# Optimization experiments

Hardware: AMD Instinct MI355X
Metric: run time of the kernel (lower is better)

Reference implementation:

```python
import jax, jax.numpy as jnp
import numpy as np
from jax import lax

ORDER = 6
WN = 0.5 / 50.0          # highpass_cutoff / (orig_fs/2)
UP, DOWN = 16, 25        # 64/100 reduced by gcd 4 (scipy resample_poly)
HALF_LEN = 10 * DOWN     # scipy kaiser half length = 10*max_rate
NTAPS = 2 * HALF_LEN + 1
PADLEN = 21              # sosfiltfilt default: 3*(2*n_sections+1), 3 biquads
CHANNELS = np.array([126, 125, 48, 112, 67, 93, 10, 61, 39, 108])
D_MODEL = 16
LN_EPS = 1e-5


def _butter_hp_sos(order, wn):
    # scipy.signal.butter(order, wn, btype='high', output='sos') in pure numpy
    fs = 2.0
    warped = 2.0 * fs * np.tan(np.pi * wn / fs)
    m = np.arange(-order + 1, order, 2)
    p = -np.exp(1j * np.pi * m / (2 * order))     # analog LP prototype poles
    k = np.real(1.0 / np.prod(-p))                # lp2hp gain (no zeros)
    p = warped / p                                # lp2hp poles; zeros at s=0
    z = np.zeros(order)
    fs2 = 2.0 * fs                                # bilinear, fs=2
    k = k * np.real(np.prod(fs2 - z) / np.prod(fs2 - p))
    z = (fs2 + z) / (fs2 - z)                     # digital zeros, all +1
    p = (fs2 + p) / (fs2 - p)
    pp = p[np.imag(p) > 0]
    pp = pp[np.argsort(-np.abs(np.abs(pp) - 1.0))]  # closest to unit circle last
    sos = []
    for i, pi in enumerate(pp):
        b = np.array([1.0, -2.0, 1.0]) * (k if i == 0 else 1.0)
        a = np.array([1.0, -2.0 * pi.real, np.abs(pi) ** 2])
        sos.append(np.concatenate([b, a]))
    return np.array(sos)


def _sosfilt_zi(sos):
    # scipy.signal.sosfilt_zi: steady-state of step response per section
    n = sos.shape[0]
    zi = np.zeros((n, 2))
    scale = 1.0
    for s in range(n):
        b0, b1, b2, _, a1, a2 = sos[s]
        A = np.array([[1.0 + a1, -1.0], [a2, 1.0]])
        B = np.array([b1 - a1 * b0, b2 - a2 * b0])
        zi[s] = scale * np.linalg.solve(A, B)
        scale *= (b0 + b1 + b2) / (1.0 + a1 + a2)
    return zi


SOS = _butter_hp_sos(ORDER, WN)
ZI = _sosfilt_zi(SOS)


def _resample_fir():
    # scipy firwin(2*half_len+1, 1/max_rate, window=('kaiser',5.0)) * up
    fc = 1.0 / DOWN
    m = np.arange(NTAPS) - (NTAPS - 1) / 2.0
    h = fc * np.sinc(fc * m) * np.kaiser(NTAPS, 5.0)
    h /= h.sum()
    return h * UP


H_BASE = _resample_fir()


def _pos_encoding(max_len, d):
    pos = np.arange(max_len)[:, None].astype(np.float64)
    div = np.exp(np.arange(0, d, 2) * (-np.log(10000.0) / d))
    pe = np.zeros((max_len, d))
    pe[:, 0::2] = np.sin(pos * div)
    pe[:, 1::2] = np.cos(pos * div)
    return pe.astype(np.float32)


PE = _pos_encoding(3840, D_MODEL)


def _sosfilt(x, zi):
    # x: (N,T), zi: (N,3,2). Cascade of biquads, transposed direct form II.
    sos = jnp.asarray(SOS, x.dtype)
    nsec = SOS.shape[0]

    def step(z, xt):
        v = xt
        zs = []
        for s in range(nsec):  # fixed tiny cascade, unrolled inside scan
            b0, b1, b2, a1, a2 = sos[s, 0], sos[s, 1], sos[s, 2], sos[s, 4], sos[s, 5]
            y = b0 * v + z[s][0]
            zs.append((b1 * v - a1 * y + z[s][1], b2 * v - a2 * y))
            v = y
        return tuple(zs), v

    z0 = tuple((zi[:, s, 0], zi[:, s, 1]) for s in range(nsec))
    _, y = lax.scan(step, z0, x.T)
    return y.T


def _sosfiltfilt(x):
    # scipy.signal.sosfiltfilt with default odd padding, padlen=21
    zi = jnp.asarray(ZI, x.dtype)
    front = 2.0 * x[:, :1] - x[:, PADLEN:0:-1]
    back = 2.0 * x[:, -1:] - x[:, -2:-PADLEN - 2:-1]
    ext = jnp.concatenate([front, x, back], axis=1)
    y = _sosfilt(ext, zi[None] * ext[:, 0, None, None])
    y = y[:, ::-1]
    y = _sosfilt(y, zi[None] * y[:, 0, None, None])
    return y[:, ::-1][:, PADLEN:-PADLEN]


def _resample_poly(x):
    # scipy.signal.resample_poly(x, 64, 100): upfirdn via dilated conv
    T = x.shape[-1]
    n_out = (T * UP) // DOWN + int((T * UP) % DOWN != 0)
    n_pre_pad = DOWN - HALF_LEN % DOWN
    n_pre_remove = (HALF_LEN + n_pre_pad) // DOWN

    def outlen(lh):
        return (((T - 1) * UP + lh) - 1) // DOWN + 1

    n_post = 0
    while outlen(NTAPS + n_pre_pad + n_post) < n_out + n_pre_remove:
        n_post += 1
    h = np.concatenate([np.zeros(n_pre_pad), H_BASE, np.zeros(n_post)])
    L = h.size
    rhs = jnp.asarray(h[::-1].copy(), x.dtype).reshape(1, 1, L)
    y = lax.conv_general_dilated(x[:, None, :], rhs, window_strides=(DOWN,),
                                 padding=[(L - 1, L - 1)], lhs_dilation=(UP,),
                                 dimension_numbers=('NCH', 'OIH', 'NCH'))
    return y[:, 0, n_pre_remove:n_pre_remove + n_out]


def _ln(x, g, b):
    mu = x.mean(-1, keepdims=True)
    var = ((x - mu) ** 2).mean(-1, keepdims=True)
    return (x - mu) * lax.rsqrt(var + LN_EPS) * g + b


def setup_inputs() -> dict:
    key = jax.random.key(0)
    ks = jax.random.split(key, 20)
    f32 = jnp.float32
    d = {
        'x': jax.random.normal(ks[0], (64, 128, 2000), f32),
        'conv_w': jax.random.normal(ks[1], (16, 10, 3), f32) * 0.15,
        'conv_b': jnp.zeros((16,), f32),
        'ln0_g': jnp.ones((16,), f32), 'ln0_b': jnp.zeros((16,), f32),
        'wqkv': jax.random.normal(ks[2], (48, 16), f32) * 0.125,
        'bqkv': jnp.zeros((48,), f32),
        'wo': jax.random.normal(ks[3], (16, 16), f32) * 0.25,
        'bo': jnp.zeros((16,), f32),
        'w1': jax.random.normal(ks[4], (32, 16), f32) * 0.2,
        'b1': jnp.zeros((32,), f32),
        'w2': jax.random.normal(ks[5], (16, 32), f32) * 0.2,
        'b2': jnp.zeros((16,), f32),
        'ln1_g': jnp.ones((16,), f32), 'ln1_b': jnp.zeros((16,), f32),
        'ln2_g': jnp.ones((16,), f32), 'ln2_b': jnp.zeros((16,), f32),
        'wfc': jax.random.normal(ks[6], (1, 16), f32) * 0.3,
        'bfc': jnp.zeros((1,), f32),
    }
    return d


def reference(x, conv_w, conv_b, ln0_g, ln0_b, wqkv, bqkv, wo, bo,
              w1, b1, w2, b2, ln1_g, ln1_b, ln2_g, ln2_b, wfc, bfc):
    B = x.shape[0]
    # remove Cz (last channel) then gather interesting channels
    x = x[:, :-1, :][:, jnp.asarray(CHANNELS), :]        # (B,10,T)
    x = x - x.mean(axis=1, keepdims=True)                # CAR
    C, T = x.shape[1], x.shape[2]
    xf = _sosfiltfilt(x.reshape(B * C, T))               # zero-phase highpass
    xr = _resample_poly(xf)                              # 100 Hz -> 64 Hz
    x = xr.reshape(B, C, -1)
    x = jnp.tanh(x)                                      # artifact_scale = 1.0
    mean = x.mean(axis=2, keepdims=True)                 # zscore, unbiased std
    var = ((x - mean) ** 2).sum(axis=2, keepdims=True) / (x.shape[2] - 1)
    std = jnp.maximum(jnp.sqrt(var), 1e-6)
    x = (x - mean) / std
    # conv1d k=3 pad=1 (10 -> 16) + relu
    x = lax.conv_general_dilated(x, conv_w, (1,), [(1, 1)],
                                 dimension_numbers=('NCH', 'OIH', 'NCH'))
    x = jax.nn.relu(x + conv_b[None, :, None])
    x = x.transpose(0, 2, 1)                             # (B,S,16)
    x = _ln(x, ln0_g, ln0_b)
    x = x + jnp.asarray(PE[:x.shape[1]], x.dtype)[None]
    # TransformerEncoderLayer, post-norm, nhead=1, relu FFN (eval: no dropout)
    qkv = x @ wqkv.T + bqkv
    q, k, v = jnp.split(qkv, 3, axis=-1)
    att = jax.nn.softmax(jnp.einsum('bqd,bkd->bqk', q, k) * 0.25, axis=-1)
    a = jnp.einsum('bqk,bkd->bqd', att, v) @ wo.T + bo
    x = _ln(x + a, ln1_g, ln1_b)
    f = jax.nn.relu(x @ w1.T + b1) @ w2.T + b2
    x = _ln(x + f, ln2_g, ln2_b)
    pooled = x.mean(axis=1)                              # adaptive avg pool -> 1
    return pooled @ wfc.T + bfc                          # (B,1)
```

## Files before the change

### kernel.cpp

```cpp
#include <hip/hip_runtime.h>
#include <cmath>
#include <complex>
#include <algorithm>

#ifndef M_PI
#define M_PI 3.14159265358979323846
#endif

typedef _Float16 f16x8 __attribute__((ext_vector_type(8)));
typedef _Float16 f16x4 __attribute__((ext_vector_type(4)));
typedef float f32x4 __attribute__((ext_vector_type(4)));

struct FiltArg {
  double b0[3], b1[3], b2[3], a1[3], a2[3];
  double zi0[3], zi1[3];
};
struct CorArg { double CA[32 * 6]; };
struct EigArg {
  double Pm[36], Pinv[36];
  double czi[6];
  double lam_re[3], lam_im[3];
  double lami_re[3], lami_im[3];
};
struct FirArg { float h[526]; };

static void design_sos(FiltArg& sa) {
  const int order = 6;
  const double wn = 0.5 / 50.0;
  const double fs = 2.0;
  double warped = 2.0 * fs * std::tan(M_PI * wn / fs);
  std::complex<double> p[6];
  for (int i = 0; i < order; i++) {
    int m = -order + 1 + 2 * i;
    p[i] = -std::exp(std::complex<double>(0.0, M_PI * m / (2.0 * order)));
  }
  std::complex<double> prod1(1, 0);
  for (int i = 0; i < 6; i++) prod1 *= -p[i];
  double k = (1.0 / prod1).real();
  for (int i = 0; i < 6; i++) p[i] = warped / p[i];
  const double fs2 = 2.0 * fs;
  std::complex<double> num(1, 0), den(1, 0);
  for (int i = 0; i < 6; i++) { num *= fs2; den *= (fs2 - p[i]); }
  k *= (num / den).real();
  for (int i = 0; i < 6; i++) p[i] = (fs2 + p[i]) / (fs2 - p[i]);
  std::complex<double> pp[3]; int n = 0;
  for (int i = 0; i < 6; i++) if (p[i].imag() > 0) pp[n++] = p[i];
  std::stable_sort(pp, pp + 3,
    [](const std::complex<double>& A, const std::complex<double>& B) {
      return std::fabs(std::abs(A) - 1.0) > std::fabs(std::abs(B) - 1.0);
    });
  double sos[3][6];
  for (int s = 0; s < 3; s++) {
    double g = (s == 0) ? k : 1.0;
    sos[s][0] = g; sos[s][1] = -2.0 * g; sos[s][2] = g;
    sos[s][3] = 1.0; sos[s][4] = -2.0 * pp[s].real(); sos[s][5] = std::norm(pp[s]);
  }
  double scale = 1.0;
  for (int s = 0; s < 3; s++) {
    double b0 = sos[s][0], b1 = sos[s][1], b2 = sos[s][2];
    double a1 = sos[s][4], a2 = sos[s][5];
    double det = 1.0 + a1 + a2;
    double r0 = b1 - a1 * b0, r1 = b2 - a2 * b0;
    double z0 = (r0 + r1) / det;
    double z1 = ((1.0 + a1) * r1 - a2 * r0) / det;
    sa.b0[s] = b0; sa.b1[s] = b1; sa.b2[s] = b2; sa.a1[s] = a1; sa.a2[s] = a2;
    sa.zi0[s] = scale * z0; sa.zi1[s] = scale * z1;
    scale *= (b0 + b1 + b2) / (1.0 + a1 + a2);
  }
}

static double host_step(const FiltArg& c, double z[6], double v) {
  for (int s = 0; s < 3; s++) {
    double y = c.b0[s] * v + z[2 * s];
    z[2 * s]     = c.b1[s] * v - c.a1[s] * y + z[2 * s + 1];
    z[2 * s + 1] = c.b2[s] * v - c.a2[s] * y;
    v = y;
  }
  return v;
}

static void build_filt(FiltArg& c, CorArg& co) {
  design_sos(c);
  for (int j = 0; j < 6; j++) {
    double z[6] = {0, 0, 0, 0, 0, 0};
    z[j] = 1.0;
    for (int i = 0; i < 32; i++) co.CA[i * 6 + j] = host_step(c, z, 0.0);
  }
}

static void build_eig(const FiltArg& c, EigArg& e) {
  double Pr[36];
  for (int s = 0; s < 3; s++) {
    double a1 = c.a1[s], a2 = c.a2[s];
    std::complex<double> disc = std::sqrt(std::complex<double>(a1 * a1 - 4.0 * a2, 0.0));
    std::complex<double> p = (-a1 + disc) / 2.0;
    if (p.imag() < 0) p = std::conj(p);
    std::complex<double> v[6] = {0, 0, 0, 0, 0, 0};
    v[2 * s] = 1.0;
    v[2 * s + 1] = a1 + p;
    std::complex<double> y = 1.0;
    for (int j = s + 1; j < 3; j++) {
      double b0j = c.b0[j], b1j = c.b1[j], b2j = c.b2[j];
      double a1j = c.a1[j], a2j = c.a2[j];
      std::complex<double> det = p * p + a1j * p + a2j;
      std::complex<double> r0 = (b1j - a1j * b0j) * y;
      std::complex<double> r1 = (b2j - a2j * b0j) * y;
      std::complex<double> z0 = (p * r0 + r1) / det;
      std::complex<double> z1 = ((p + a1j) * r1 - a2j * r0) / det;
      v[2 * j] = z0; v[2 * j + 1] = z1;
      y = b0j * y + z0;
    }
    for (int i = 0; i < 6; i++) {
      Pr[i * 6 + 2 * s]     = v[i].real();
      Pr[i * 6 + 2 * s + 1] = v[i].imag();
    }
    std::complex<double> lam = std::pow(p, 32);
    e.lam_re[s] = lam.real(); e.lam_im[s] = lam.imag();
    std::complex<double> li = 1.0 / lam;
    e.lami_re[s] = li.real(); e.lami_im[s] = li.imag();
  }
  for (int i = 0; i < 36; i++) e.Pm[i] = Pr[i];
  double M[6][12];
  for (int i = 0; i < 6; i++)
    for (int j = 0; j < 6; j++) { M[i][j] = Pr[i * 6 + j]; M[i][6 + j] = (i == j) ? 1.0 : 0.0; }
  for (int col = 0; col < 6; col++) {
    int piv = col;
    for (int i = col + 1; i < 6; i++)
      if (std::fabs(M[i][col]) > std::fabs(M[piv][col])) piv = i;
    if (piv != col) for (int j = 0; j < 12; j++) std::swap(M[col][j], M[piv][j]);
    double d = M[col][col];
    for (int j = 0; j < 12; j++) M[col][j] /= d;
    for (int i = 0; i < 6; i++) if (i != col) {
      double f = M[i][col];
      for (int j = 0; j < 12; j++) M[i][j] -= f * M[col][j];
    }
  }
  for (int i = 0; i < 6; i++)
    for (int j = 0; j < 6; j++) e.Pinv[i * 6 + j] = M[i][6 + j];
  double zv[6];
  for (int s = 0; s < 3; s++) { zv[2 * s] = c.zi0[s]; zv[2 * s + 1] = c.zi1[s]; }
  for (int i = 0; i < 6; i++) {
    double sum = 0.0;
    for (int j = 0; j < 6; j++) sum += e.Pinv[i * 6 + j] * zv[j];
    e.czi[i] = sum;
  }
}

static double bessel_i0(double x) {
  double s = 1.0, t = 1.0;
  for (int k = 1; k < 64; k++) {
    double u = x / (2.0 * k);
    t *= u * u; s += t;
    if (t < 1e-18 * s) break;
  }
  return s;
}

static void design_fir(FirArg& fa) {
  double h[501];
  const double fc = 1.0 / 25.0;
  double denom = bessel_i0(5.0);
  double sum = 0.0;
  for (int nn = 0; nn < 501; nn++) {
    double m = nn - 250.0;
    double xx = fc * m;
    double snc = (nn == 250) ? 1.0 : std::sin(M_PI * xx) / (M_PI * xx);
    double r = (2.0 * nn) / 500.0 - 1.0;
    double w = bessel_i0(5.0 * std::sqrt(std::max(0.0, 1.0 - r * r))) / denom;
    h[nn] = fc * snc * w; sum += h[nn];
  }
  for (int nn = 0; nn < 25; nn++) fa.h[nn] = 0.0f;
  for (int nn = 0; nn < 501; nn++) fa.h[25 + nn] = (float)(h[nn] / sum * 16.0);
}

__device__ inline double waveReduceSum(double v) {
  #pragma unroll
  for (int off = 32; off > 0; off >>= 1) v += __shfl_down(v, off, 64);
  return v;
}

__device__ inline void cpow_int(double br, double bi, int n, double& rr_, double& ri_) {
  double rr = 1.0, ri = 0.0;
  while (n) {
    if (n & 1) { double t = rr * br - ri * bi; ri = rr * bi + ri * br; rr = t; }
    double t2 = br * br - bi * bi; bi = 2.0 * br * bi; br = t2;
    n >>= 1;
  }
  rr_ = rr; ri_ = ri;
}

__global__ __launch_bounds__(256) void k_chansel_pe(const float* __restrict__ x,
                                                    float* __restrict__ xs,
                                                    float* __restrict__ pe,
                                                    float* __restrict__ out) {
  int gid = blockIdx.x;
  if (gid < 500) {
    int idx = gid * 256 + threadIdx.x;
    int b = idx / 2000, t = idx % 2000;
    const int ch[10] = {126, 125, 48, 112, 67, 93, 10, 61, 39, 108};
    const float* xb = x + (size_t)b * 128 * 2000;
    float v[10]; float s = 0.f;
    #pragma unroll
    for (int c = 0; c < 10; c++) { v[c] = xb[ch[c] * 2000 + t]; s += v[c]; }
    s *= 0.1f;
    #pragma unroll
    for (int c = 0; c < 10; c++) xs[((size_t)b * 10 + c) * 2000 + t] = v[c] - s;
  } else {
    int i = (gid - 500) * 256 + threadIdx.x;
    int t = i >> 4, d = i & 15, j = d >> 1;
    double div = exp(-((double)(2 * j)) * 0.5756462732485114);
    double a = (double)t * div;
    pe[i] = (float)((d & 1) ? cos(a) : sin(a));
    if (gid == 579 && threadIdx.x < 64) out[threadIdx.x] = 0.f;
  }
}

#define XR(t) xr[(t) + ((t) >> 5)]
#define YF(t) yf[(t) + ((t) >> 5)]
__global__ __launch_bounds__(64) void k_filtfilt(float* __restrict__ xs,
                                                 FiltArg c, CorArg co, EigArg eg) {
  __shared__ float xr[2112];
  __shared__ double yf[2112];
  int r = blockIdx.x;
  int k = threadIdx.x;
  float* x = xs + (size_t)r * 2000;

  float x0f = x[0], xlf = x[1999];
  for (int t = k; t < 2048; t += 64) {
    float v;
    if (t < 21)        v = 2.f * x0f - x[21 - t];
    else if (t < 2021) v = x[t - 21];
    else if (t < 2042) v = 2.f * xlf - x[4019 - t];
    else               v = 0.f;
    XR(t) = v;
  }
  __syncthreads();

  double b0[3], b1[3], b2[3], a1[3], a2[3];
  #pragma unroll
  for (int s = 0; s < 3; s++) {
    b0[s] = c.b0[s]; b1[s] = c.b1[s]; b2[s] = c.b2[s];
    a1[s] = c.a1[s]; a2[s] = c.a2[s];
  }
  auto step = [&](double* z, double v) -> double {
    #pragma unroll
    for (int s = 0; s < 3; s++) {
      double y = b0[s] * v + z[2 * s];
      z[2 * s]     = b1[s] * v - a1[s] * y + z[2 * s + 1];
      z[2 * s + 1] = b2[s] * v - a2[s] * y;
      v = y;
    }
    return v;
  };

  auto eigscan = [&](double seed, const double* F, double* zst) {
    double G[6];
    #pragma unroll
    for (int i = 0; i < 6; i++) {
      double s = 0.0;
      #pragma unroll
      for (int j = 0; j < 6; j++) s += eg.Pinv[i * 6 + j] * F[j];
      G[i] = s;
    }
    double coord[6];
    #pragma unroll
    for (int s3 = 0; s3 < 3; s3++) {
      double gre = G[2 * s3], gim = -G[2 * s3 + 1];
      double mre, mim;
      cpow_int(eg.lami_re[s3], eg.lami_im[s3], k, mre, mim);
      double tre = mre * gre - mim * gim;
      double tim = mre * gim + mim * gre;
      double sre = tre, sim = tim;
      #pragma unroll
      for (int off = 1; off < 64; off <<= 1) {
        double ore = __shfl_up(sre, off, 64);
        double oim = __shfl_up(sim, off, 64);
        sre += (k >= off) ? ore : 0.0;
        sim += (k >= off) ? oim : 0.0;
      }
      double Sre = sre - tre, Sim = sim - tim;
      double c0re = seed * eg.czi[2 * s3];
      double c0im = -seed * eg.czi[2 * s3 + 1];
      double lkre, lkim;
      cpow_int(eg.lam_re[s3], eg.lam_im[s3], k, lkre, lkim);
      double lm1re = lkre * eg.lami_re[s3] - lkim * eg.lami_im[s3];
      double lm1im = lkre * eg.lami_im[s3] + lkim * eg.lami_re[s3];
      if (k == 0) { lm1re = 0.0; lm1im = 0.0; }
      double cre = lkre * c0re - lkim * c0im + lm1re * Sre - lm1im * Sim;
      double cim = lkre * c0im + lkim * c0re + lm1re * Sim + lm1im * Sre;
      coord[2 * s3] = cre;
      coord[2 * s3 + 1] = -cim;
    }
    #pragma unroll
    for (int i = 0; i < 6; i++) {
      double s = 0.0;
      #pragma unroll
      for (int j = 0; j < 6; j++) s += eg.Pm[i * 6 + j] * coord[j];
      zst[i] = s;
    }
  };

  int t0 = k * 32;
  double z[6], yreg[32], zst[6];

  #pragma unroll
  for (int i = 0; i < 6; i++) z[i] = 0.0;
  for (int i = 0; i < 32; i++) yreg[i] = step(z, (double)XR(t0 + i));
  eigscan((double)XR(0), z, zst);
  for (int i = 0; i < 32; i++) {
    double corr = 0.0;
    #pragma unroll
    for (int j = 0; j < 6; j++) corr += co.CA[i * 6 + j] * zst[j];
    YF(t0 + i) = yreg[i] + corr;
  }
  __syncthreads();

  auto rin = [&](int j) -> double { return (j <= 2041) ? YF(2041 - j) : 0.0; };
  double seedB = YF(2041);
  #pragma unroll
  for (int i = 0; i < 6; i++) z[i] = 0.0;
  for (int i = 0; i < 32; i++) yreg[i] = step(z, rin(t0 + i));
  eigscan(seedB, z, zst);
  for (int i = 0; i < 32; i++) {
    int j = t0 + i;
    if (j >= 21 && j <= 2020) {
      double corr = 0.0;
      #pragma unroll
      for (int jj = 0; jj < 6; jj++) corr += co.CA[i * 6 + jj] * zst[jj];
      x[2020 - j] = (float)(yreg[i] + corr);
    }
  }
}

__global__ __launch_bounds__(256) void k_resample_norm(const float* __restrict__ xf,
                                                       float* __restrict__ xn,
                                                       FirArg fa) {
  __shared__ float xl[2000];
  __shared__ float hl[526];
  int r = blockIdx.x;
  const float* x = xf + (size_t)r * 2000;
  for (int i = threadIdx.x; i < 2000; i += 256) xl[i] = x[i];
  for (int i = threadIdx.x; i < 526; i += 256) hl[i] = fa.h[i];
  __syncthreads();
  float vals[5];
  #pragma unroll
  for (int kk = 0; kk < 5; kk++) {
    int o = threadIdx.x + kk * 256;
    int P = 25 * (o + 11);
    int phase = P & 15;
    float acc = 0.f;
    for (int m = phase; m <= 525; m += 16) {
      int idx = (P - m) >> 4;
      if (idx >= 0 && idx < 2000) acc += hl[m] * xl[idx];
    }
    vals[kk] = tanhf(acc);
  }
  double s = 0.0, ss = 0.0;
  #pragma unroll
  for (int kk = 0; kk < 5; kk++) {
    s += (double)vals[kk]; ss += (double)vals[kk] * (double)vals[kk];
  }
  s = waveReduceSum(s); ss = waveReduceSum(ss);
  __shared__ double red[8];
  int wid = threadIdx.x >> 6, lane = threadIdx.x & 63;
  if (lane == 0) { red[wid] = s; red[4 + wid] = ss; }
  __syncthreads();
  double S = red[0] + red[1] + red[2] + red[3];
  double SS = red[4] + red[5] + red[6] + red[7];
  double mean = S / 1280.0;
  double var = (SS - 1280.0 * mean * mean) / 1279.0;
  double sd = fmax(sqrt(fmax(var, 0.0)), 1e-6);
  float fmean = (float)mean, finv = (float)(1.0 / sd);
  #pragma unroll
  for (int kk = 0; kk < 5; kk++)
    xn[(size_t)r * 1280 + threadIdx.x + kk * 256] = (vals[kk] - fmean) * finv;
}

__global__ __launch_bounds__(256) void k_conv_ln_pe_qkv(const float* __restrict__ xn,
    const float* __restrict__ cw, const float* __restrict__ cb,
    const float* __restrict__ g0, const float* __restrict__ bt0,
    const float* __restrict__ wqkv, const float* __restrict__ bqkv,
    const float* __restrict__ pe,
    float* __restrict__ x0,
    float* __restrict__ Q, float* __restrict__ K, float* __restrict__ V) {
  __shared__ float w[480], bias[16], gg[16], gb[16];
  __shared__ float wq[768], bq[48];
  for (int i = threadIdx.x; i < 480; i += 256) w[i] = cw[i];
  for (int i = threadIdx.x; i < 768; i += 256) wq[i] = wqkv[i];
  if (threadIdx.x < 16) {
    bias[threadIdx.x] = cb[threadIdx.x];
    gg[threadIdx.x] = g0[threadIdx.x];
    gb[threadIdx.x] = bt0[threadIdx.x];
  }
  if (threadIdx.x < 48) bq[threadIdx.x] = bqkv[threadIdx.x];
  __syncthreads();
  int idx = blockIdx.x * 256 + threadIdx.x;
  int b = idx / 1280, t = idx % 1280;
  const float* xb = xn + (size_t)b * 10 * 1280;
  float in[10][3];
  #pragma unroll
  for (int i = 0; i < 10; i++)
    #pragma unroll
    for (int k = 0; k < 3; k++) {
      int tt = t - 1 + k;
      in[i][k] = (tt >= 0 && tt < 1280) ? xb[i * 1280 + tt] : 0.f;
    }
  float o[16];
  #pragma unroll
  for (int oc = 0; oc < 16; oc++) {
    float a = bias[oc];
    #pragma unroll
    for (int i = 0; i < 10; i++)
      #pragma unroll
      for (int k = 0; k < 3; k++) a += in[i][k] * w[oc * 30 + i * 3 + k];
    o[oc] = fmaxf(a, 0.f);
  }
  float mu = 0.f;
  #pragma unroll
  for (int d = 0; d < 16; d++) mu += o[d];
  mu *= (1.f / 16.f);
  float var = 0.f;
  #pragma unroll
  for (int d = 0; d < 16; d++) { float dd = o[d] - mu; var += dd * dd; }
  var *= (1.f / 16.f);
  float inv = 1.f / sqrtf(var + 1e-5f);
  float xv[16];
  float* outp = x0 + (size_t)idx * 16;
  const float* pep = pe + t * 16;
  #pragma unroll
  for (int d = 0; d < 16; d++) {
    xv[d] = (o[d] - mu) * inv * gg[d] + gb[d] + pep[d];
    outp[d] = xv[d];
  }
  float* qp = Q + (size_t)idx * 16;
  float* kp = K + (size_t)idx * 16;
  float* vp = V + (size_t)idx * 16;
  #pragma unroll
  for (int j = 0; j < 16; j++) {
    float a = bq[j];
    #pragma unroll
    for (int d = 0; d < 16; d++) a += xv[d] * wq[j * 16 + d];
    qp[j] = a;
  }
  #pragma unroll
  for (int j = 0; j < 16; j++) {
    float a = bq[16 + j];
    #pragma unroll
    for (int d = 0; d < 16; d++) a += xv[d] * wq[(16 + j) * 16 + d];
    kp[j] = a;
  }
  #pragma unroll
  for (int j = 0; j < 16; j++) {
    float a = bq[32 + j];
    #pragma unroll
    for (int d = 0; d < 16; d++) a += xv[d] * wq[(32 + j) * 16 + d];
    vp[j] = a;
  }
}

#define ATT_SHIFT 12.0f
__global__ __launch_bounds__(256) void k_attn_mfma(const float* __restrict__ Q,
    const float* __restrict__ K, const float* __restrict__ V,
    float* __restrict__ A) {
  __shared__ __align__(16) _Float16 Ks[64 * 40];
  __shared__ __align__(16) _Float16 Vt[16 * 72];
  __shared__ __align__(16) _Float16 Pld[4][16 * 40];
  int tid = threadIdx.x;
  int b  = blockIdx.x / 20;
  int rg = blockIdx.x % 20;
  int wv = tid >> 6;
  int lane = tid & 63;
  int col = lane & 15;
  int quad = lane >> 4;
  size_t base = (size_t)b * 1280;
  int row0 = rg * 64 + wv * 16;

  f16x8 qf;
  #pragma unroll
  for (int j = 0; j < 8; j++) qf[j] = (_Float16)0.f;
  if (quad < 2) {
    const float* qp = Q + (base + row0 + col) * 16 + quad * 8;
    #pragma unroll
    for (int j = 0; j < 8; j++) qf[j] = (_Float16)(0.25f * qp[j]);
  }
  f32x4 oacc = {0.f, 0.f, 0.f, 0.f};
  float lacc = 0.f;

  for (int s = 0; s < 20; s++) {
    __syncthreads();
    {
      int key = tid >> 2, part = tid & 3;
      const float* kp = K + (base + s * 64 + key) * 16 + part * 4;
      f16x4 hk, hz;
      #pragma unroll
      for (int j = 0; j < 4; j++) { hk[j] = (_Float16)kp[j]; hz[j] = (_Float16)0.f; }
      *(f16x4*)&Ks[key * 40 + part * 4] = hk;
      *(f16x4*)&Ks[key * 40 + 16 + part * 4] = hz;
      const float* vp = V + (base + s * 64 + key) * 16 + part * 4;
      #pragma unroll
      for (int j = 0; j < 4; j++) Vt[(part * 4 + j) * 72 + key] = (_Float16)vp[j];
    }
    __syncthreads();
    #pragma unroll
    for (int c = 0; c < 2; c++) {
      #pragma unroll
      for (int t = 0; t < 2; t++) {
        int keyoff = c * 32 + t * 16;
        f16x8 af = *(f16x8*)&Ks[(keyoff + col) * 40 + quad * 8];
        f32x4 sf = {0.f, 0.f, 0.f, 0.f};
        sf = __builtin_amdgcn_mfma_f32_16x16x32_f16(af, qf, sf, 0, 0, 0);
        f16x4 ph;
        float psum = 0.f;
        #pragma unroll
        for (int r = 0; r < 4; r++) {
          float p = __expf(sf[r] - ATT_SHIFT);
          psum += p;
          ph[r] = (_Float16)p;
        }
        lacc += psum;
        *(f16x4*)&Pld[wv][col * 40 + t * 16 + quad * 4] = ph;
      }
      __syncthreads();
      f16x8 pf = *(f16x8*)&Pld[wv][col * 40 + quad * 8];
      f16x8 vf = *(f16x8*)&Vt[col * 72 + c * 32 + quad * 8];
      oacc = __builtin_amdgcn_mfma_f32_16x16x32_f16(pf, vf, oacc, 0, 0, 0);
      __syncthreads();
    }
  }
  lacc += __shfl_xor(lacc, 16, 64);
  lacc += __shfl_xor(lacc, 32, 64);
  #pragma unroll
  for (int r = 0; r < 4; r++) {
    float lr = __shfl(lacc, quad * 4 + r, 64);
    A[(base + row0 + quad * 4 + r) * 16 + col] = oacc[r] / lr;
  }
}

__global__ __launch_bounds__(256) void k_combine_pool(
    const float* __restrict__ A, const float* __restrict__ x0,
    const float* __restrict__ wo, const float* __restrict__ bo,
    const float* __restrict__ w1, const float* __restrict__ b1,
    const float* __restrict__ w2, const float* __restrict__ b2,
    const float* __restrict__ g1, const float* __restrict__ bb1,
    const float* __restrict__ g2, const float* __restrict__ bb2,
    const float* __restrict__ wfc, const float* __restrict__ bfc,
    float* __restrict__ out) {
  __shared__ float swo[256], sw1[512], sw2[512];
  __shared__ float sbo[16], sb1[32], sb2[16], sg1[16], sbb1[16], sg2[16], sbb2[16];
  __shared__ float swf[16];
  int tid = threadIdx.x;
  swo[tid] = wo[tid];
  for (int i = tid; i < 512; i += 256) { sw1[i] = w1[i]; sw2[i] = w2[i]; }
  if (tid < 16) {
    sbo[tid] = bo[tid]; sb2[tid] = b2[tid];
    sg1[tid] = g1[tid]; sbb1[tid] = bb1[tid];
    sg2[tid] = g2[tid]; sbb2[tid] = bb2[tid];
    swf[tid] = wfc[tid];
  }
  if (tid < 32) sb1[tid] = b1[tid];
  __syncthreads();

  int idx = blockIdx.x * 256 + tid;
  int bb = blockIdx.x / 5;
  const float* pa = A + (size_t)idx * 16;
  float a[16];
  #pragma unroll
  for (int d = 0; d < 16; d++) a[d] = pa[d];
  float h[16];
  const float* xr = x0 + (size_t)idx * 16;
  #pragma unroll
  for (int d = 0; d < 16; d++) {
    float o = sbo[d];
    #pragma unroll
    for (int e = 0; e < 16; e++) o += a[e] * swo[d * 16 + e];
    h[d] = xr[d] + o;
  }
  float mu = 0.f;
  #pragma unroll
  for (int d = 0; d < 16; d++) mu += h[d];
  mu *= (1.f / 16.f);
  float var = 0.f;
  #pragma unroll
  for (int d = 0; d < 16; d++) { float dd = h[d] - mu; var += dd * dd; }
  var *= (1.f / 16.f);
  float inv = 1.f / sqrtf(var + 1e-5f);
  float x1[16];
  #pragma unroll
  for (int d = 0; d < 16; d++) x1[d] = (h[d] - mu) * inv * sg1[d] + sbb1[d];
  float t1[32];
  #pragma unroll
  for (int j = 0; j < 32; j++) {
    float u = sb1[j];
    #pragma unroll
    for (int d = 0; d < 16; d++) u += x1[d] * sw1[j * 16 + d];
    t1[j] = fmaxf(u, 0.f);
  }
  float h2[16];
  #pragma unroll
  for (int d = 0; d < 16; d++) {
    float u = sb2[d];
    #pragma unroll
    for (int j = 0; j < 32; j++) u += t1[j] * sw2[d * 32 + j];
    h2[d] = x1[d] + u;
  }
  mu = 0.f;
  #pragma unroll
  for (int d = 0; d < 16; d++) mu += h2[d];
  mu *= (1.f / 16.f);
  var = 0.f;
  #pragma unroll
  for (int d = 0; d < 16; d++) { float dd = h2[d] - mu; var += dd * dd; }
  var *= (1.f / 16.f);
  inv = 1.f / sqrtf(var + 1e-5f);
  float pv = 0.f;
  #pragma unroll
  for (int d = 0; d < 16; d++)
    pv += ((h2[d] - mu) * inv * sg2[d] + sbb2[d]) * swf[d];
  double part = waveReduceSum((double)pv);
  __shared__ double red[4];
  int wid = tid >> 6, lane = tid & 63;
  if (lane == 0) red[wid] = part;
  __syncthreads();
  if (tid == 0) {
    double S = red[0] + red[1] + red[2] + red[3];
    float add = (float)(S / 1280.0);
    if (blockIdx.x % 5 == 0) add += bfc[0];
    atomicAdd(&out[bb], add);
  }
}

extern "C" void kernel_launch(void* const* d_in, const int* in_sizes, int n_in,
                              void* d_out, int out_size, void* d_ws, size_t ws_size,
                              hipStream_t stream) {
  const float* x    = (const float*)d_in[0];
  const float* cw   = (const float*)d_in[1];
  const float* cb   = (const float*)d_in[2];
  const float* g0   = (const float*)d_in[3];
  const float* bt0  = (const float*)d_in[4];
  const float* wqkv = (const float*)d_in[5];
  const float* bqkv = (const float*)d_in[6];
  const float* wo   = (const float*)d_in[7];
  const float* bo   = (const float*)d_in[8];
  const float* w1   = (const float*)d_in[9];
  const float* b1   = (const float*)d_in[10];
  const float* w2   = (const float*)d_in[11];
  const float* b2   = (const float*)d_in[12];
  const float* g1   = (const float*)d_in[13];
  const float* bb1  = (const float*)d_in[14];
  const float* g2   = (const float*)d_in[15];
  const float* bb2  = (const float*)d_in[16];
  const float* wfc  = (const float*)d_in[17];
  const float* bfc  = (const float*)d_in[18];
  float* out = (float*)d_out;

  float* ws = (float*)d_ws;
  float* xs = ws;
  float* y1 = xs + 1280000;
  float* xn = y1 + 1306880;
  float* x0 = xn + 819200;
  float* Q  = x0 + 1310720;
  float* Kb = Q  + 1310720;
  float* Vb = Kb + 1310720;
  float* pe = Vb + 1310720;
  float* Abuf = ws;

  FiltArg fc; CorArg co; EigArg eg; FirArg fa;
  build_filt(fc, co);
  build_eig(fc, eg);
  design_fir(fa);

  k_chansel_pe<<<580, 256, 0, stream>>>(x, xs, pe, out);
  k_filtfilt<<<640, 64, 0, stream>>>(xs, fc, co, eg);
  k_resample_norm<<<640, 256, 0, stream>>>(xs, xn, fa);
  k_conv_ln_pe_qkv<<<320, 256, 0, stream>>>(xn, cw, cb, g0, bt0, wqkv, bqkv,
                                            pe, x0, Q, Kb, Vb);
  k_attn_mfma<<<1280, 256, 0, stream>>>(Q, Kb, Vb, Abuf);
  k_combine_pool<<<320, 256, 0, stream>>>(Abuf, x0, wo, bo, w1, b1, w2, b2,
                                          g1, bb1, g2, bb2, wfc, bfc, out);
}
```

Baseline: 252.5 us.

## Split filtfilt scan across two waves with 16-sample chunks per thread

The parallel IIR filtfilt kernel now uses 128 threads per row instead of 64, and each thread handles 16 samples instead of 32. The eigen-basis chunk scan becomes a two-wave scan: each wave runs a shuffle prefix and wave 1 adds wave 0's total through shared memory. The host precomputes the correction table and eigenvalue powers for the 16-sample chunk length. This shortens each thread's serial fp64 recurrence and raises parallelism, at the cost of an extra block barrier and more complex-power work per chunk.

```diff
diff --git a/kernel.cpp b/kernel.cpp
--- a/kernel.cpp
+++ b/kernel.cpp
@@ -15,7 +15,7 @@
   double b0[3], b1[3], b2[3], a1[3], a2[3];
   double zi0[3], zi1[3];
 };
-struct CorArg { double CA[32 * 6]; };
+struct CorArg { double CA[16 * 6]; };
 struct EigArg {
   double Pm[36], Pinv[36];
   double czi[6];
@@ -84,7 +84,7 @@
   for (int j = 0; j < 6; j++) {
     double z[6] = {0, 0, 0, 0, 0, 0};
     z[j] = 1.0;
-    for (int i = 0; i < 32; i++) co.CA[i * 6 + j] = host_step(c, z, 0.0);
+    for (int i = 0; i < 16; i++) co.CA[i * 6 + j] = host_step(c, z, 0.0);
   }
 }
 
@@ -114,7 +114,7 @@
       Pr[i * 6 + 2 * s]     = v[i].real();
       Pr[i * 6 + 2 * s + 1] = v[i].imag();
     }
-    std::complex<double> lam = std::pow(p, 32);
+    std::complex<double> lam = std::pow(p, 16);
     e.lam_re[s] = lam.real(); e.lam_im[s] = lam.imag();
     std::complex<double> li = 1.0 / lam;
     e.lami_re[s] = li.real(); e.lami_im[s] = li.imag();
@@ -217,16 +217,19 @@
 
 #define XR(t) xr[(t) + ((t) >> 5)]
 #define YF(t) yf[(t) + ((t) >> 5)]
-__global__ __launch_bounds__(64) void k_filtfilt(float* __restrict__ xs,
-                                                 FiltArg c, CorArg co, EigArg eg) {
+__global__ __launch_bounds__(128) void k_filtfilt(float* __restrict__ xs,
+                                                  FiltArg c, CorArg co, EigArg eg) {
   __shared__ float xr[2112];
   __shared__ double yf[2112];
+  __shared__ double wsum[3][2];
   int r = blockIdx.x;
-  int k = threadIdx.x;
+  int gk = threadIdx.x;
+  int lane = gk & 63;
+  int wv = gk >> 6;
   float* x = xs + (size_t)r * 2000;
 
   float x0f = x[0], xlf = x[1999];
-  for (int t = k; t < 2048; t += 64) {
+  for (int t = gk; t < 2048; t += 128) {
     float v;
     if (t < 21)        v = 2.f * x0f - x[21 - t];
     else if (t < 2021) v = x[t - 21];
@@ -262,30 +265,39 @@
       for (int j = 0; j < 6; j++) s += eg.Pinv[i * 6 + j] * F[j];
       G[i] = s;
     }
-    double coord[6];
+    double tre[3], tim[3], sre[3], sim[3];
     #pragma unroll
     for (int s3 = 0; s3 < 3; s3++) {
       double gre = G[2 * s3], gim = -G[2 * s3 + 1];
       double mre, mim;
-      cpow_int(eg.lami_re[s3], eg.lami_im[s3], k, mre, mim);
-      double tre = mre * gre - mim * gim;
-      double tim = mre * gim + mim * gre;
-      double sre = tre, sim = tim;
+      cpow_int(eg.lami_re[s3], eg.lami_im[s3], gk, mre, mim);
+      tre[s3] = mre * gre - mim * gim;
+      tim[s3] = mre * gim + mim * gre;
+      double pr = tre[s3], pi = tim[s3];
       #pragma unroll
       for (int off = 1; off < 64; off <<= 1) {
-        double ore = __shfl_up(sre, off, 64);
-        double oim = __shfl_up(sim, off, 64);
-        sre += (k >= off) ? ore : 0.0;
-        sim += (k >= off) ? oim : 0.0;
+        double ore = __shfl_up(pr, off, 64);
+        double oim = __shfl_up(pi, off, 64);
+        pr += (lane >= off) ? ore : 0.0;
+        pi += (lane >= off) ? oim : 0.0;
       }
-      double Sre = sre - tre, Sim = sim - tim;
+      sre[s3] = pr; sim[s3] = pi;
+      if (wv == 0 && lane == 63) { wsum[s3][0] = pr; wsum[s3][1] = pi; }
+    }
+    __syncthreads();
+    double coord[6];
+    #pragma unroll
+    for (int s3 = 0; s3 < 3; s3++) {
+      double inc_re = sre[s3] + (wv ? wsum[s3][0] : 0.0);
+      double inc_im = sim[s3] + (wv ? wsum[s3][1] : 0.0);
+      double Sre = inc_re - tre[s3], Sim = inc_im - tim[s3];
       double c0re = seed * eg.czi[2 * s3];
       double c0im = -seed * eg.czi[2 * s3 + 1];
       double lkre, lkim;
-      cpow_int(eg.lam_re[s3], eg.lam_im[s3], k, lkre, lkim);
+      cpow_int(eg.lam_re[s3], eg.lam_im[s3], gk, lkre, lkim);
       double lm1re = lkre * eg.lami_re[s3] - lkim * eg.lami_im[s3];
       double lm1im = lkre * eg.lami_im[s3] + lkim * eg.lami_re[s3];
-      if (k == 0) { lm1re = 0.0; lm1im = 0.0; }
+      if (gk == 0) { lm1re = 0.0; lm1im = 0.0; }
       double cre = lkre * c0re - lkim * c0im + lm1re * Sre - lm1im * Sim;
       double cim = lkre * c0im + lkim * c0re + lm1re * Sim + lm1im * Sre;
       coord[2 * s3] = cre;
@@ -300,14 +312,14 @@
     }
   };
 
-  int t0 = k * 32;
-  double z[6], yreg[32], zst[6];
+  int t0 = gk * 16;
+  double z[6], yreg[16], zst[6];
 
   #pragma unroll
   for (int i = 0; i < 6; i++) z[i] = 0.0;
-  for (int i = 0; i < 32; i++) yreg[i] = step(z, (double)XR(t0 + i));
+  for (int i = 0; i < 16; i++) yreg[i] = step(z, (double)XR(t0 + i));
   eigscan((double)XR(0), z, zst);
-  for (int i = 0; i < 32; i++) {
+  for (int i = 0; i < 16; i++) {
     double corr = 0.0;
     #pragma unroll
     for (int j = 0; j < 6; j++) corr += co.CA[i * 6 + j] * zst[j];
@@ -319,9 +331,9 @@
   double seedB = YF(2041);
   #pragma unroll
   for (int i = 0; i < 6; i++) z[i] = 0.0;
-  for (int i = 0; i < 32; i++) yreg[i] = step(z, rin(t0 + i));
+  for (int i = 0; i < 16; i++) yreg[i] = step(z, rin(t0 + i));
   eigscan(seedB, z, zst);
-  for (int i = 0; i < 32; i++) {
+  for (int i = 0; i < 16; i++) {
     int j = t0 + i;
     if (j >= 21 && j <= 2020) {
       double corr = 0.0;
@@ -670,7 +682,7 @@
   design_fir(fa);
 
   k_chansel_pe<<<580, 256, 0, stream>>>(x, xs, pe, out);
-  k_filtfilt<<<640, 64, 0, stream>>>(xs, fc, co, eg);
+  k_filtfilt<<<640, 128, 0, stream>>>(xs, fc, co, eg);
   k_resample_norm<<<640, 256, 0, stream>>>(xs, xn, fa);
   k_conv_ln_pe_qkv<<<320, 256, 0, stream>>>(xn, cw, cb, g0, bt0, wqkv, bqkv,
                                             pe, x0, Q, Kb, Vb);
```

After: 242.8 us. 1.04x faster.
